# Performance work log

Hardware: AMD Instinct MI355X
Metric: run time of the kernel (lower is better)

Reference implementation:

```python
import jax, jax.numpy as jnp
import numpy as np

TOPK = 30  # from init_kwargs


def setup_inputs() -> dict:
    key = jax.random.key(0)
    k1, k2, k3 = jax.random.split(key, 3)
    BH, N, D = 32, 2048, 64  # (batch*heads, seq_len, head_dim)
    return {
        "q": jax.random.normal(k1, (BH, N, D), dtype=jnp.float32),
        "k": jax.random.normal(k2, (BH, N, D), dtype=jnp.float32),
        "v": jax.random.normal(k3, (BH, N, D), dtype=jnp.float32),
        "B": 2048,          # == seq_len N (used for mask shape in original)
        "num_heads": 8,     # unused by the math, kept for signature parity
    }


def reference(q, k, v, B, num_heads):
    # scores: [BH, N, N]  (torch.bmm(q, k.transpose(1,2)))
    scores = jnp.einsum('bnd,bmd->bnm', q, k)
    # scale=None and attn_mask=None in the default call -> both branches skipped
    BH, N, _ = scores.shape
    # top-k per row, scatter 1.0 into a zero mask (faithful to torch.scatter_)
    _, idx = jax.lax.top_k(scores, TOPK)                      # [BH, N, TOPK]
    bi = jnp.arange(BH)[:, None, None]
    ri = jnp.arange(N)[None, :, None]
    keep = jnp.zeros((BH, N, N), dtype=bool).at[bi, ri, idx].set(True)
    # masked softmax over last axis (dim=2)
    masked = jnp.where(keep, scores, -jnp.inf)
    attn = jax.nn.softmax(masked, axis=-1)
    # dropout p=0.0 -> identity
    context = jnp.einsum('bnm,bmd->bnd', attn, v)
    return context, attn
```

## Files before the change

### kernel.cpp

```cpp
#include <hip/hip_runtime.h>
#include <hip/hip_bf16.h>

#define BHn 32
#define Nn 2048
#define Dn 64
#define KSEL 30
#define CAP 92
#define RB 32
#define CT 64
#define ZTH 1.90f

typedef short bf16x8 __attribute__((ext_vector_type(8)));
typedef float f32x4 __attribute__((ext_vector_type(4)));
typedef unsigned long long u64;

__device__ __forceinline__ unsigned ford(float x) {
  unsigned b = __float_as_uint(x);
  return (b & 0x80000000u) ? ~b : (b | 0x80000000u);
}
__device__ __forceinline__ float unford(unsigned u) {
  unsigned b = (u & 0x80000000u) ? (u & 0x7fffffffu) : ~u;
  return __uint_as_float(b);
}
__device__ __forceinline__ u64 umax64(u64 a, u64 b) { return a > b ? a : b; }

__device__ __forceinline__ void split2(float a, float b, ushort2& hi, ushort2& lo) {
  __hip_bfloat162 h = __float22bfloat162_rn(make_float2(a, b));
  union { __hip_bfloat162 v; ushort2 u; } ch; ch.v = h;
  hi = ch.u;
  float2 hf = __bfloat1622float2(h);
  __hip_bfloat162 l = __float22bfloat162_rn(make_float2(a - hf.x, b - hf.y));
  union { __hip_bfloat162 v; ushort2 u; } cl; cl.v = l;
  lo = cl.u;
}

__device__ __forceinline__ void pack8(float4 x0, float4 x1, bf16x8& hi, bf16x8& lo) {
  ushort2 h0, l0, h1, l1, h2, l2, h3, l3;
  split2(x0.x, x0.y, h0, l0); split2(x0.z, x0.w, h1, l1);
  split2(x1.x, x1.y, h2, l2); split2(x1.z, x1.w, h3, l3);
  hi = (bf16x8){(short)h0.x, (short)h0.y, (short)h1.x, (short)h1.y,
                (short)h2.x, (short)h2.y, (short)h3.x, (short)h3.y};
  lo = (bf16x8){(short)l0.x, (short)l0.y, (short)l1.x, (short)l1.y,
                (short)l2.x, (short)l2.y, (short)l3.x, (short)l3.y};
}

__global__ __launch_bounds__(256, 4) void score_select(
    const float* __restrict__ q, const float* __restrict__ k,
    const float* __restrict__ v, float* __restrict__ ctx,
    float* __restrict__ attn, unsigned* __restrict__ flags) {
  __shared__ ushort kh[CT][64], kl[CT][64];
  __shared__ u64 candL[RB][CAP];
  __shared__ unsigned ccnt[RB];
  __shared__ float tf[RB];

  const int t = threadIdx.x;
  const int bid = blockIdx.x;
  const int bh = (bid & 7) * 4 + ((bid >> 3) & 3);
  const int rb = bid >> 5;
  const int lane = t & 63, w = t >> 6;
  const int m16 = lane & 15, quad = lane >> 4;
  const int wc = w;

  const float* qb = q + ((size_t)bh * Nn + rb * RB) * Dn;
  const float* kb = k + (size_t)bh * Nn * Dn;
  const size_t growbase = (size_t)bh * Nn + (size_t)rb * RB;

  bf16x8 qaH[2][2], qaL[2][2];
#pragma unroll
  for (int ks = 0; ks < 2; ++ks)
#pragma unroll
    for (int mt = 0; mt < 2; ++mt) {
      const float* p = qb + (mt * 16 + m16) * Dn + (ks * 4 + quad) * 8;
      float4 x0 = *(const float4*)p;
      float4 x1 = *(const float4*)(p + 4);
      pack8(x0, x1, qaH[ks][mt], qaL[ks][mt]);
    }

  if (t < RB) {
    const float* qr = qb + t * Dn;
    float ss = 0.f;
#pragma unroll
    for (int i = 0; i < 16; ++i) {
      float4 a = *(const float4*)(qr + i * 4);
      ss = fmaf(a.x, a.x, ss); ss = fmaf(a.y, a.y, ss);
      ss = fmaf(a.z, a.z, ss); ss = fmaf(a.w, a.w, ss);
    }
    tf[t] = ZTH * sqrtf(ss);
    ccnt[t] = 0u;
  }

  float4 pre[4];
#pragma unroll
  for (int i = 0; i < 4; ++i) {
    int c = t + 256 * i;
    pre[i] = *(const float4*)(kb + (size_t)(c >> 4) * Dn + (c & 15) * 4);
  }
  __syncthreads();

  unsigned tfr[2][4];
#pragma unroll
  for (int mt = 0; mt < 2; ++mt)
#pragma unroll
    for (int rg = 0; rg < 4; ++rg)
      tfr[mt][rg] = ford(tf[mt * 16 + quad * 4 + rg]);

  const f32x4 Z = (f32x4){0.f, 0.f, 0.f, 0.f};

  for (int ct = 0; ct < Nn / CT; ++ct) {
#pragma unroll
    for (int i = 0; i < 4; ++i) {
      int c = t + 256 * i;
      int row = c >> 4, f4 = c & 15;
      float4 a = pre[i];
      int sp = (((f4 >> 1) ^ (row & 7)) << 1) | (f4 & 1);
      ushort2 h0, l0, h1, l1;
      split2(a.x, a.y, h0, l0);
      split2(a.z, a.w, h1, l1);
      *(ushort4*)&kh[row][sp * 4] = make_ushort4(h0.x, h0.y, h1.x, h1.y);
      *(ushort4*)&kl[row][sp * 4] = make_ushort4(l0.x, l0.y, l1.x, l1.y);
    }
    __syncthreads();

    if (ct + 1 < Nn / CT) {
#pragma unroll
      for (int i = 0; i < 4; ++i) {
        int c = t + 256 * i;
        pre[i] = *(const float4*)(kb + (size_t)((ct + 1) * CT + (c >> 4)) * Dn + (c & 15) * 4);
      }
    }

    {
      int zr = w * 8 + (ct >> 3);
      float* ab = attn + (growbase + zr) * (size_t)Nn + (ct & 7) * 256 + lane * 4;
      __builtin_nontemporal_store(Z, (f32x4*)ab);
    }

    f32x4 acc[2];
#pragma unroll
    for (int mt = 0; mt < 2; ++mt) acc[mt] = (f32x4){0.f, 0.f, 0.f, 0.f};

#pragma unroll
    for (int ks = 0; ks < 2; ++ks) {
      int rr = wc * 16 + m16;
      int ch = (ks * 4 + quad) ^ (rr & 7);
      bf16x8 bH = *(const bf16x8*)&kh[rr][ch * 8];
      bf16x8 bL = *(const bf16x8*)&kl[rr][ch * 8];
#pragma unroll
      for (int mt = 0; mt < 2; ++mt) {
        acc[mt] = __builtin_amdgcn_mfma_f32_16x16x32_bf16(qaL[ks][mt], bH, acc[mt], 0, 0, 0);
        acc[mt] = __builtin_amdgcn_mfma_f32_16x16x32_bf16(qaH[ks][mt], bL, acc[mt], 0, 0, 0);
        acc[mt] = __builtin_amdgcn_mfma_f32_16x16x32_bf16(qaH[ks][mt], bH, acc[mt], 0, 0, 0);
      }
    }

#pragma unroll
    for (int mt = 0; mt < 2; ++mt)
#pragma unroll
      for (int rg = 0; rg < 4; ++rg) {
        unsigned tk = tfr[mt][rg];
        int rl = mt * 16 + quad * 4 + rg;
        float s = acc[mt][rg];
        unsigned fk = ford(s);
        if (fk > tk) {
          unsigned pos = atomicAdd(&ccnt[rl], 1u);
          if (pos < CAP) {
            int col = ct * CT + wc * 16 + m16;
            candL[rl][pos] = ((u64)fk << 32) | (unsigned)(2047 - col);
          }
        }
      }
    __syncthreads();
  }

  const float* vb = v + (size_t)bh * Nn * Dn;

  for (int i = 0; i < RB / 4; ++i) {
    const int rl = w * (RB / 4) + i;
    const size_t gr = growbase + rl;
    const int C = (int)ccnt[rl];
    const bool bad = (C < KSEL) || (C > CAP);
    if (lane == 0) flags[gr] = bad ? 1u : 0u;

    if (!bad) {
      u64* sw_ = &candL[rl][0];
      const int slots = (C + 63) >> 6;
      u64 mykey[2] = {0ull, 0ull};
      int rk[2] = {CAP, CAP};
      float es[2] = {0.f, 0.f};
      u64 mymax = 0ull;
#pragma unroll
      for (int tt = 0; tt < 2; ++tt) {
        if (tt < slots) {
          int p = lane + 64 * tt;
          mykey[tt] = (p < C) ? sw_[p] : 0ull;
          mymax = umax64(mymax, mykey[tt]);
        }
      }
#pragma unroll
      for (int off = 32; off; off >>= 1) mymax = umax64(mymax, __shfl_xor(mymax, off));
      const float mrow = unford((unsigned)(mymax >> 32));

#pragma unroll 1
      for (int tt = 0; tt < slots; ++tt) {
        int r = 0;
        u64 me = mykey[tt];
        for (int jj = 0; jj < C; ++jj) r += (sw_[jj] > me);
        rk[tt] = r;
      }
      float z = 0.f;
#pragma unroll
      for (int tt = 0; tt < 2; ++tt) {
        int p = lane + 64 * tt;
        bool sel = (tt < slots) && (p < C) && (rk[tt] < KSEL);
        es[tt] = sel ? __expf(unford((unsigned)(mykey[tt] >> 32)) - mrow) : 0.f;
        z += es[tt];
      }
#pragma unroll
      for (int off = 32; off; off >>= 1) z += __shfl_xor(z, off);
      const float invZ = 1.f / z;

#pragma unroll
      for (int tt = 0; tt < 2; ++tt) {
        int p = lane + 64 * tt;
        if (tt < slots && p < C && rk[tt] < KSEL) {
          float wt = es[tt] * invZ;
          int col = 2047 - (int)(mykey[tt] & 0xffffffffu);
          sw_[rk[tt]] = ((u64)__float_as_uint(wt) << 32) | (unsigned)col;
        }
      }
      float a = 0.f;
#pragma unroll
      for (int p = 0; p < KSEL; ++p) {
        u64 e = sw_[p];
        a = fmaf(__uint_as_float((unsigned)(e >> 32)), vb[(e & 0x7ffull) * Dn + lane], a);
      }
      ctx[gr * Dn + lane] = a;
    }
  }

  asm volatile("s_waitcnt vmcnt(0)" ::: "memory");

#pragma unroll 1
  for (int i = 0; i < RB / 4; ++i) {
    const int rl = w * (RB / 4) + i;
    const size_t gr = growbase + rl;
    const int C = (int)ccnt[rl];
    if (C >= KSEL && C <= CAP && lane < KSEL) {
      u64 e = candL[rl][lane];
      float wt = __uint_as_float((unsigned)(e >> 32));
      int col = (int)(e & 0x7ffull);
      __builtin_nontemporal_store(wt, attn + gr * (size_t)Nn + col);
    }
  }
}

__global__ __launch_bounds__(256) void repair_rows(
    const float* __restrict__ q, const float* __restrict__ k,
    const float* __restrict__ v, float* __restrict__ ctx,
    float* __restrict__ attn, const unsigned* __restrict__ flags) {
  __shared__ float sc2[Nn];
  __shared__ u64 red[256];
  __shared__ float qrow[Dn];
  __shared__ int selc[KSEL];
  __shared__ float selv[KSEL];
  __shared__ float zsh;
  __shared__ unsigned flagbuf[256];

  const int t = threadIdx.x;
  const int base = blockIdx.x * 256;
  flagbuf[t] = flags[base + t];
  __syncthreads();

  for (int i = 0; i < 256; ++i) {
    if (flagbuf[i] == 0u) continue;
    const int gr = base + i;
    const int bh = gr >> 11;
    if (t < Dn) qrow[t] = q[(size_t)gr * Dn + t];
    __syncthreads();
    const float* kb = k + (size_t)bh * Nn * Dn;
#pragma unroll
    for (int j = 0; j < 8; ++j) {
      int col = t + 256 * j;
      float s = 0.f;
      for (int d = 0; d < Dn; d += 4) {
        float4 kk = *(const float4*)(kb + (size_t)col * Dn + d);
        s = fmaf(qrow[d], kk.x, s);
        s = fmaf(qrow[d + 1], kk.y, s);
        s = fmaf(qrow[d + 2], kk.z, s);
        s = fmaf(qrow[d + 3], kk.w, s);
      }
      sc2[col] = s;
    }
    __syncthreads();
    for (int p = 0; p < KSEL; ++p) {
      u64 best = 0ull;
#pragma unroll
      for (int j = 0; j < 8; ++j) {
        int col = t + 256 * j;
        u64 kk = ((u64)ford(sc2[col]) << 32) | (unsigned)(2047 - col);
        best = umax64(best, kk);
      }
      red[t] = best;
      __syncthreads();
      for (int off = 128; off; off >>= 1) {
        if (t < off) red[t] = umax64(red[t], red[t + off]);
        __syncthreads();
      }
      if (t == 0) {
        u64 b = red[0];
        int col = 2047 - (int)(b & 0xffffffffu);
        selc[p] = col;
        selv[p] = unford((unsigned)(b >> 32));
        sc2[col] = -3.4e38f;
      }
      __syncthreads();
    }
    if (t == 0) {
      float m = selv[0], zz = 0.f;
      for (int p = 0; p < KSEL; ++p) zz += __expf(selv[p] - m);
      zsh = 1.f / zz;
    }
    __syncthreads();
    if (t < KSEL)
      attn[(size_t)gr * Nn + selc[t]] = __expf(selv[t] - selv[0]) * zsh;
    if (t < Dn) {
      const float* vb = v + (size_t)bh * Nn * Dn;
      float a = 0.f;
      for (int p = 0; p < KSEL; ++p)
        a = fmaf(__expf(selv[p] - selv[0]) * zsh, vb[(size_t)selc[p] * Dn + t], a);
      ctx[(size_t)gr * Dn + t] = a;
    }
    __syncthreads();
  }
}

extern "C" void kernel_launch(void* const* d_in, const int* in_sizes, int n_in,
                              void* d_out, int out_size, void* d_ws,
                              size_t ws_size, hipStream_t stream) {
  const float* q = (const float*)d_in[0];
  const float* k = (const float*)d_in[1];
  const float* v = (const float*)d_in[2];
  float* out = (float*)d_out;
  float* ctx = out;
  float* attn = out + (size_t)BHn * Nn * Dn;

  unsigned* flags = (unsigned*)d_ws;

  score_select<<<dim3(BHn * Nn / RB), 256, 0, stream>>>(q, k, v, ctx, attn, flags);
  repair_rows<<<dim3(BHn * Nn / 256), 256, 0, stream>>>(q, k, v, ctx, attn, flags);
}
```

Baseline: 781.9 us.

## Load K fragments directly into registers, dropping LDS staging and per-tile barriers

Each wave now loads its own K rows straight from global memory into registers in MFMA fragment layout and splits them into bf16 hi/lo there, instead of staging the tile through swizzled shared memory. This removes the LDS writes and reads and the two __syncthreads per column tile. A two-buffer register ping-pong prefetches the next tile while the current one is processed, and the zero-fill of attn is reorganised into two stores per iteration. The cost is more register use and global loads that are less coalesced, since each lane reads a strided 32-byte piece.

```diff
diff --git a/kernel.cpp b/kernel.cpp
--- a/kernel.cpp
+++ b/kernel.cpp
@@ -8,6 +8,7 @@
 #define CAP 92
 #define RB 32
 #define CT 64
+#define NT_TILES (Nn / CT)
 #define ZTH 1.90f
 
 typedef short bf16x8 __attribute__((ext_vector_type(8)));
@@ -48,7 +49,6 @@
     const float* __restrict__ q, const float* __restrict__ k,
     const float* __restrict__ v, float* __restrict__ ctx,
     float* __restrict__ attn, unsigned* __restrict__ flags) {
-  __shared__ ushort kh[CT][64], kl[CT][64];
   __shared__ u64 candL[RB][CAP];
   __shared__ unsigned ccnt[RB];
   __shared__ float tf[RB];
@@ -88,13 +88,6 @@
     tf[t] = ZTH * sqrtf(ss);
     ccnt[t] = 0u;
   }
-
-  float4 pre[4];
-#pragma unroll
-  for (int i = 0; i < 4; ++i) {
-    int c = t + 256 * i;
-    pre[i] = *(const float4*)(kb + (size_t)(c >> 4) * Dn + (c & 15) * 4);
-  }
   __syncthreads();
 
   unsigned tfr[2][4];
@@ -106,51 +99,42 @@
 
   const f32x4 Z = (f32x4){0.f, 0.f, 0.f, 0.f};
 
-  for (int ct = 0; ct < Nn / CT; ++ct) {
-#pragma unroll
-    for (int i = 0; i < 4; ++i) {
-      int c = t + 256 * i;
-      int row = c >> 4, f4 = c & 15;
-      float4 a = pre[i];
-      int sp = (((f4 >> 1) ^ (row & 7)) << 1) | (f4 & 1);
-      ushort2 h0, l0, h1, l1;
-      split2(a.x, a.y, h0, l0);
-      split2(a.z, a.w, h1, l1);
-      *(ushort4*)&kh[row][sp * 4] = make_ushort4(h0.x, h0.y, h1.x, h1.y);
-      *(ushort4*)&kl[row][sp * 4] = make_ushort4(l0.x, l0.y, l1.x, l1.y);
-    }
-    __syncthreads();
-
-    if (ct + 1 < Nn / CT) {
-#pragma unroll
-      for (int i = 0; i < 4; ++i) {
-        int c = t + 256 * i;
-        pre[i] = *(const float4*)(kb + (size_t)((ct + 1) * CT + (c >> 4)) * Dn + (c & 15) * 4);
-      }
-    }
-
+  const float* kl0 = kb + ((size_t)wc * 16 + m16) * Dn + quad * 8;
+
+  auto LOADT = [&](int ct, float4* buf) {
+    const float* p = kl0 + (size_t)ct * CT * Dn;
+    buf[0] = *(const float4*)(p);
+    buf[1] = *(const float4*)(p + 4);
+    buf[2] = *(const float4*)(p + 32);
+    buf[3] = *(const float4*)(p + 36);
+  };
+
+  auto PROC = [&](int ct, float4* buf) {
     {
-      int zr = w * 8 + (ct >> 3);
-      float* ab = attn + (growbase + zr) * (size_t)Nn + (ct & 7) * 256 + lane * 4;
+      float* ab = attn + (growbase + w * 8 + (ct >> 2)) * (size_t)Nn +
+                  (ct & 3) * 512 + lane * 4;
       __builtin_nontemporal_store(Z, (f32x4*)ab);
-    }
+      __builtin_nontemporal_store(Z, (f32x4*)(ab + 256));
+    }
+
+    bf16x8 bH0, bL0, bH1, bL1;
+    pack8(buf[0], buf[1], bH0, bL0);
+    pack8(buf[2], buf[3], bH1, bL1);
 
     f32x4 acc[2];
 #pragma unroll
     for (int mt = 0; mt < 2; ++mt) acc[mt] = (f32x4){0.f, 0.f, 0.f, 0.f};
-
-#pragma unroll
-    for (int ks = 0; ks < 2; ++ks) {
-      int rr = wc * 16 + m16;
-      int ch = (ks * 4 + quad) ^ (rr & 7);
-      bf16x8 bH = *(const bf16x8*)&kh[rr][ch * 8];
-      bf16x8 bL = *(const bf16x8*)&kl[rr][ch * 8];
-#pragma unroll
-      for (int mt = 0; mt < 2; ++mt) {
-        acc[mt] = __builtin_amdgcn_mfma_f32_16x16x32_bf16(qaL[ks][mt], bH, acc[mt], 0, 0, 0);
-        acc[mt] = __builtin_amdgcn_mfma_f32_16x16x32_bf16(qaH[ks][mt], bL, acc[mt], 0, 0, 0);
-        acc[mt] = __builtin_amdgcn_mfma_f32_16x16x32_bf16(qaH[ks][mt], bH, acc[mt], 0, 0, 0);
-      }
+#pragma unroll
+    for (int mt = 0; mt < 2; ++mt) {
+      acc[mt] = __builtin_amdgcn_mfma_f32_16x16x32_bf16(qaL[0][mt], bH0, acc[mt], 0, 0, 0);
+      acc[mt] = __builtin_amdgcn_mfma_f32_16x16x32_bf16(qaH[0][mt], bL0, acc[mt], 0, 0, 0);
+      acc[mt] = __builtin_amdgcn_mfma_f32_16x16x32_bf16(qaH[0][mt], bH0, acc[mt], 0, 0, 0);
+    }
+#pragma unroll
+    for (int mt = 0; mt < 2; ++mt) {
+      acc[mt] = __builtin_amdgcn_mfma_f32_16x16x32_bf16(qaL[1][mt], bH1, acc[mt], 0, 0, 0);
+      acc[mt] = __builtin_amdgcn_mfma_f32_16x16x32_bf16(qaH[1][mt], bL1, acc[mt], 0, 0, 0);
+      acc[mt] = __builtin_amdgcn_mfma_f32_16x16x32_bf16(qaH[1][mt], bH1, acc[mt], 0, 0, 0);
     }
 
 #pragma unroll
@@ -169,8 +153,18 @@
           }
         }
       }
-    __syncthreads();
-  }
+  };
+
+  float4 bufA[4], bufB[4];
+  LOADT(0, bufA);
+#pragma unroll 1
+  for (int ct = 0; ct < NT_TILES; ct += 2) {
+    if (ct + 1 < NT_TILES) LOADT(ct + 1, bufB);
+    PROC(ct, bufA);
+    if (ct + 2 < NT_TILES) LOADT(ct + 2, bufA);
+    PROC(ct + 1, bufB);
+  }
+  __syncthreads();
 
   const float* vb = v + (size_t)bh * Nn * Dn;
 
```

Measured after the change: 827.1 us. 1.06x slower.
